# Performance work log

Measured on AMD Instinct MI355X. Metric: run time of the kernel, lower is better.

The kernel has to match this reference:

```python
import jax, jax.numpy as jnp
import numpy as np

N_NODES = 100000
N_EDGES = 1600000
IN_F = 16
C1, C2 = 32, 64
HID = 128
N_CLASSES = 10
NUM_LAYERS = 3


def setup_inputs() -> dict:
    key = jax.random.key(0)
    ks = jax.random.split(key, 20)
    s = 0.1
    inp = {
        "x": jax.random.normal(ks[0], (N_NODES, IN_F), dtype=jnp.float32),
        "edge_index": jax.random.randint(ks[1], (2, N_EDGES), 0, N_NODES, dtype=jnp.int64),
        "edge_attr": jax.random.uniform(ks[2], (N_EDGES, 1), dtype=jnp.float32),
        # conv1 (out=32): per-step weight [L, 32, 32], GRUCell params
        "W1": jax.random.normal(ks[3], (NUM_LAYERS, C1, C1), dtype=jnp.float32) * s,
        "Wih1": jax.random.normal(ks[4], (3 * C1, C1), dtype=jnp.float32) * s,
        "Whh1": jax.random.normal(ks[5], (3 * C1, C1), dtype=jnp.float32) * s,
        "bih1": jnp.zeros((3 * C1,), dtype=jnp.float32),
        "bhh1": jnp.zeros((3 * C1,), dtype=jnp.float32),
        # conv2 (out=64)
        "W2": jax.random.normal(ks[6], (NUM_LAYERS, C2, C2), dtype=jnp.float32) * s,
        "Wih2": jax.random.normal(ks[7], (3 * C2, C2), dtype=jnp.float32) * s,
        "Whh2": jax.random.normal(ks[8], (3 * C2, C2), dtype=jnp.float32) * s,
        "bih2": jnp.zeros((3 * C2,), dtype=jnp.float32),
        "bhh2": jnp.zeros((3 * C2,), dtype=jnp.float32),
        # MLP head
        "fc1_w": jax.random.normal(ks[9], (HID, C2), dtype=jnp.float32) * s,
        "fc1_b": jnp.zeros((HID,), dtype=jnp.float32),
        "fc2_w": jax.random.normal(ks[10], (N_CLASSES, HID), dtype=jnp.float32) * s,
        "fc2_b": jnp.zeros((N_CLASSES,), dtype=jnp.float32),
    }
    return inp


def _gru_cell(m, h, Wih, Whh, bih, bhh):
    gi = m @ Wih.T + bih
    gh = h @ Whh.T + bhh
    ir, iz, inn = jnp.split(gi, 3, axis=1)
    hr, hz, hn = jnp.split(gh, 3, axis=1)
    r = jax.nn.sigmoid(ir + hr)
    z = jax.nn.sigmoid(iz + hz)
    n = jnp.tanh(inn + r * hn)
    return (1.0 - z) * n + z * h


def _gated_graph_conv(x, edge_index, edge_weight, W, Wih, Whh, bih, bhh):
    # PyG GatedGraphConv with aggr='max'
    n, c = x.shape
    out_ch = W.shape[-1]
    h = jnp.pad(x, ((0, 0), (0, out_ch - c))) if c < out_ch else x
    src, dst = edge_index[0], edge_index[1]
    ew = edge_weight[:, None]
    for i in range(W.shape[0]):
        m = h @ W[i]
        msg = m[src] * ew                      # [E, out_ch] gather + scale
        agg = jax.ops.segment_max(msg, dst, num_segments=n)  # scatter-max
        agg = jnp.where(jnp.isfinite(agg), agg, 0.0)         # empty segs -> 0
        h = _gru_cell(agg, h, Wih, Whh, bih, bhh)
    return h


def reference(x, edge_index, edge_attr, W1, Wih1, Whh1, bih1, bhh1,
              W2, Wih2, Whh2, bih2, bhh2, fc1_w, fc1_b, fc2_w, fc2_b):
    ew = jnp.squeeze(edge_attr)
    h = jax.nn.elu(_gated_graph_conv(x, edge_index, ew, W1, Wih1, Whh1, bih1, bhh1))
    h = jax.nn.elu(_gated_graph_conv(h, edge_index, ew, W2, Wih2, Whh2, bih2, bhh2))
    h = jax.nn.elu(h @ fc1_w.T + fc1_b)
    logits = h @ fc2_w.T + fc2_b
    return jax.nn.log_softmax(logits, axis=1)
```

## Files before the change

### kernel.cpp

```cpp
#include <hip/hip_runtime.h>
#include <math.h>

#define N_NODES 100000
#define N_EDGES 1600000
#define SCAN_BS 1024
#define NBK 8
#define BKSH 14
#define NBINS (N_NODES*NBK)

typedef __attribute__((ext_vector_type(8))) short bf8_t;
typedef __attribute__((ext_vector_type(4))) float f4_t;
typedef unsigned short us;

__device__ __forceinline__ float sigmoidf_(float x){ return 1.f/(1.f + expf(-x)); }
__device__ __forceinline__ float eluf_(float x){ return x > 0.f ? x : expm1f(x); }
__device__ __forceinline__ us f2bf(float x){
  unsigned u = __float_as_uint(x);
  unsigned r = u + 0x7FFFu + ((u>>16)&1u);
  return (us)(r>>16);
}
__device__ __forceinline__ float bf2f(us v){
  return __uint_as_float(((unsigned)v)<<16);
}

__global__ void prep_all(const float* __restrict__ Wih1, const float* __restrict__ Whh1,
                         const float* __restrict__ Wih2, const float* __restrict__ Whh2,
                         const float* __restrict__ W1,   const float* __restrict__ W2,
                         const float* __restrict__ fc1w, const float* __restrict__ fc2w,
                         const float* __restrict__ fc2b,
                         us* Wihb1, us* Whhb1, us* Wihb2, us* Whhb2,
                         us* Wtb1, us* Wtb2, us* fc1wb, us* fc2wpb, float* fc2bp){
  int i = blockIdx.x*256 + threadIdx.x;
  if (i < 3072) { Wihb1[i]=f2bf(Wih1[i]); return; } i -= 3072;
  if (i < 3072) { Whhb1[i]=f2bf(Whh1[i]); return; } i -= 3072;
  if (i < 12288){ Wihb2[i]=f2bf(Wih2[i]); return; } i -= 12288;
  if (i < 12288){ Whhb2[i]=f2bf(Whh2[i]); return; } i -= 12288;
  if (i < 3072) { int k=i%32, c=(i/32)%32, m=i/1024;
                  Wtb1[i]=f2bf(W1[m*1024 + k*32 + c]); return; } i -= 3072;
  if (i < 12288){ int k=i%64, c=(i/64)%64, m=i/4096;
                  Wtb2[i]=f2bf(W2[m*4096 + k*64 + c]); return; } i -= 12288;
  if (i < 8192) { fc1wb[i]=f2bf(fc1w[i]); return; } i -= 8192;
  if (i < 2048) { int c=i/128, k=i%128;
                  fc2wpb[i]=(c<10)?f2bf(fc2w[c*128+k]):(us)0; return; } i -= 2048;
  if (i < 16)   { fc2bp[i] = (i<10)? fc2b[i] : 0.f; }
}

__global__ void zero_counts(int* cnt, int* cur, int n){
  int i = blockIdx.x*blockDim.x + threadIdx.x;
  if (i < n){ cnt[i]=0; cur[i]=0; }
}
__global__ void count_kernel(const int* __restrict__ ei, int* __restrict__ cnt, int e){
  int i = blockIdx.x*blockDim.x + threadIdx.x;
  if (i < e){
    int s = ei[i], d = ei[N_EDGES + i];
    atomicAdd(&cnt[d*NBK + (s>>BKSH)], 1);
  }
}
__global__ void scan1_kernel(const int* __restrict__ cnt, int* __restrict__ pre,
                             int* __restrict__ bsum, int n){
  __shared__ int sh[SCAN_BS];
  int t = threadIdx.x, gi = blockIdx.x*SCAN_BS + t;
  int v = (gi < n) ? cnt[gi] : 0;
  sh[t] = v;
  __syncthreads();
  for (int off=1; off<SCAN_BS; off<<=1){
    int u = (t>=off)?sh[t-off]:0;
    __syncthreads();
    sh[t] += u;
    __syncthreads();
  }
  if (gi < n) pre[gi] = sh[t] - v;
  if (t == SCAN_BS-1) bsum[blockIdx.x] = sh[t];
}
__global__ void scan2_kernel(int* __restrict__ bsum, int nb){
  __shared__ int sh[1024];
  int t = threadIdx.x;
  int v = (t < nb) ? bsum[t] : 0;
  sh[t] = v;
  __syncthreads();
  for (int off=1; off<1024; off<<=1){
    int u = (t>=off)?sh[t-off]:0;
    __syncthreads();
    sh[t] += u;
    __syncthreads();
  }
  if (t < nb) bsum[t] = sh[t] - v;
}
__global__ void scan3_kernel(const int* __restrict__ pre, const int* __restrict__ bsum,
                             int* __restrict__ rs2, int total){
  int i = blockIdx.x*blockDim.x + threadIdx.x;
  if (i < total) rs2[i] = pre[i] + bsum[i/SCAN_BS];
  if (i == 0) rs2[total] = N_EDGES;
}
__global__ void scatter_kernel(const int* __restrict__ ei, const float* __restrict__ ea,
    const int* __restrict__ rs2, int* __restrict__ cur,
    long long* __restrict__ esrc, int e){
  int i0 = (blockIdx.x*blockDim.x + threadIdx.x)*2;
  #pragma unroll
  for (int j=0;j<2;j++){
    int i = i0 + j;
    if (i < e){
      int s = ei[i], d = ei[N_EDGES + i];
      int bin = d*NBK + (s>>BKSH);
      int p = rs2[bin] + atomicAdd(&cur[bin], 1);
      long long v = (long long)(unsigned)s
                  | ((long long)(unsigned)__float_as_int(ea[i]) << 32);
      __builtin_nontemporal_store(v, &esrc[p]);
    }
  }
}

__global__ void pad_x_kernel(const float* __restrict__ x, float* __restrict__ h,
                             us* __restrict__ hb, int n){
  int i = blockIdx.x*blockDim.x + threadIdx.x;
  if (i < n*32){
    int node = i >> 5, c = i & 31;
    float v = (c < 16) ? x[node*16 + c] : 0.f;
    h[i] = v;
    hb[i] = f2bf(v);
  }
}
__global__ void transition_kernel(const float* __restrict__ h1, float* __restrict__ h2,
                                  us* __restrict__ h2b, int n){
  int i = blockIdx.x*blockDim.x + threadIdx.x;
  if (i < n*64){
    int node = i >> 6, c = i & 63;
    float v = (c < 32) ? eluf_(h1[node*32 + c]) : 0.f;
    h2[i] = v;
    h2b[i] = f2bf(v);
  }
}

template<int C>
__global__ __launch_bounds__(256) void mgemm_mfma(const us* __restrict__ hb,
    const us* __restrict__ Wtb, us* __restrict__ mb, int n){
  constexpr int NT = C/16, KS = C/32;
  int l = threadIdx.x & 63, w = threadIdx.x >> 6;
  int mbase = blockIdx.x*64 + w*16;
  if (mbase >= n) return;
  int lr = l & 15, lk = (l >> 4)*8;
  f4_t acc[NT];
  #pragma unroll
  for (int t=0;t<NT;t++) acc[t] = f4_t{0.f,0.f,0.f,0.f};
  #pragma unroll
  for (int ks=0; ks<KS; ks++){
    int k0 = ks*32 + lk;
    bf8_t a = *(const bf8_t*)(hb + (size_t)(mbase+lr)*C + k0);
    #pragma unroll
    for (int t=0;t<NT;t++){
      bf8_t b = *(const bf8_t*)(Wtb + (size_t)(t*16+lr)*C + k0);
      acc[t] = __builtin_amdgcn_mfma_f32_16x16x32_bf16(a, b, acc[t], 0, 0, 0);
    }
  }
  int dr = (l>>4)*4;
  #pragma unroll
  for (int t=0;t<NT;t++){
    #pragma unroll
    for (int r=0;r<4;r++){
      int node = mbase + dr + r;
      if (node < n)
        mb[(size_t)node*C + t*16 + lr] = f2bf(acc[t][r]);
    }
  }
}

template<int C>
__global__ void agg_kernel(const us* __restrict__ mb, const int* __restrict__ rs2,
    const long long* __restrict__ esrc, us* __restrict__ aggb, int n_nodes){
  constexpr int GPN = C/8;
  int gid = blockIdx.x*blockDim.x + threadIdx.x;
  int nn = gid / GPN, g8 = gid % GPN;
  if (nn >= n_nodes) return;
  int s = rs2[nn*NBK], e = rs2[nn*NBK + NBK];
  float acc[8];
  #pragma unroll
  for (int j=0;j<8;j++) acc[j] = -__builtin_inff();
  const us* mbg = mb + g8*8;
  int i = s;
  for (; i+4<=e; i+=4){
    long long e0 = esrc[i], e1 = esrc[i+1], e2 = esrc[i+2], e3 = esrc[i+3];
    uint4 v0 = *(const uint4*)(mbg + (size_t)(unsigned)(e0 & 0xFFFFFFFF)*C);
    uint4 v1 = *(const uint4*)(mbg + (size_t)(unsigned)(e1 & 0xFFFFFFFF)*C);
    uint4 v2 = *(const uint4*)(mbg + (size_t)(unsigned)(e2 & 0xFFFFFFFF)*C);
    uint4 v3 = *(const uint4*)(mbg + (size_t)(unsigned)(e3 & 0xFFFFFFFF)*C);
    float w0 = __int_as_float((int)(e0>>32)), w1 = __int_as_float((int)(e1>>32));
    float w2 = __int_as_float((int)(e2>>32)), w3 = __int_as_float((int)(e3>>32));
    unsigned a0[4] = {v0.x, v0.y, v0.z, v0.w};
    unsigned a1[4] = {v1.x, v1.y, v1.z, v1.w};
    unsigned a2[4] = {v2.x, v2.y, v2.z, v2.w};
    unsigned a3[4] = {v3.x, v3.y, v3.z, v3.w};
    #pragma unroll
    for (int q=0;q<4;q++){
      float x0 = fmaxf(__uint_as_float(a0[q]<<16)*w0, __uint_as_float(a1[q]<<16)*w1);
      float x1 = fmaxf(__uint_as_float(a2[q]<<16)*w2, __uint_as_float(a3[q]<<16)*w3);
      float y0 = fmaxf(__uint_as_float(a0[q]&0xFFFF0000u)*w0, __uint_as_float(a1[q]&0xFFFF0000u)*w1);
      float y1 = fmaxf(__uint_as_float(a2[q]&0xFFFF0000u)*w2, __uint_as_float(a3[q]&0xFFFF0000u)*w3);
      acc[2*q]   = fmaxf(acc[2*q],   fmaxf(x0, x1));
      acc[2*q+1] = fmaxf(acc[2*q+1], fmaxf(y0, y1));
    }
  }
  for (; i<e; i++){
    long long e0 = esrc[i];
    uint4 v0 = *(const uint4*)(mbg + (size_t)(unsigned)(e0 & 0xFFFFFFFF)*C);
    float w0 = __int_as_float((int)(e0>>32));
    unsigned a0[4] = {v0.x, v0.y, v0.z, v0.w};
    #pragma unroll
    for (int q=0;q<4;q++){
      acc[2*q]   = fmaxf(acc[2*q],   __uint_as_float(a0[q]<<16)*w0);
      acc[2*q+1] = fmaxf(acc[2*q+1], __uint_as_float(a0[q]&0xFFFF0000u)*w0);
    }
  }
  unsigned r[8];
  #pragma unroll
  for (int j=0;j<8;j++) r[j] = (e > s) ? (unsigned)f2bf(acc[j]) : 0u;
  uint4 o;
  o.x = r[0] | (r[1]<<16); o.y = r[2] | (r[3]<<16);
  o.z = r[4] | (r[5]<<16); o.w = r[6] | (r[7]<<16);
  *(uint4*)(aggb + (size_t)nn*C + g8*8) = o;
}

template<int C, bool COMPUTE_M>
__global__ __launch_bounds__(256) void gru_mfma(
    const us* __restrict__ aggb, const us* __restrict__ hbin,
    const float* __restrict__ hfin,
    const us* __restrict__ Wihb, const us* __restrict__ Whhb,
    const float* __restrict__ bih, const float* __restrict__ bhh,
    const us* __restrict__ Wtb_next,
    float* __restrict__ hfout, us* __restrict__ hbout, us* __restrict__ mbout, int n){
  constexpr int NT = 3*C/16;
  constexpr int KS = C/32;
  constexpr int CT = C/16;
  constexpr int TST = C + 8;
  constexpr int TSZ = COMPUTE_M ? 16*TST : 1;
  __shared__ us tlds[4][TSZ];
  int l = threadIdx.x & 63, w = threadIdx.x >> 6;
  int mbase = blockIdx.x*64 + w*16;
  int lr = l & 15, lk = (l >> 4)*8;
  f4_t accI[NT], accH[NT];
  #pragma unroll
  for (int t=0;t<NT;t++){ accI[t]=f4_t{0.f,0.f,0.f,0.f}; accH[t]=f4_t{0.f,0.f,0.f,0.f}; }
  #pragma unroll
  for (int ks=0; ks<KS; ks++){
    int k0 = ks*32 + lk;
    bf8_t aI = *(const bf8_t*)(aggb + (size_t)(mbase+lr)*C + k0);
    bf8_t aH = *(const bf8_t*)(hbin + (size_t)(mbase+lr)*C + k0);
    #pragma unroll
    for (int t=0;t<NT;t++){
      bf8_t bI = *(const bf8_t*)(Wihb + (size_t)(t*16+lr)*C + k0);
      accI[t] = __builtin_amdgcn_mfma_f32_16x16x32_bf16(aI, bI, accI[t], 0, 0, 0);
      bf8_t bH = *(const bf8_t*)(Whhb + (size_t)(t*16+lr)*C + k0);
      accH[t] = __builtin_amdgcn_mfma_f32_16x16x32_bf16(aH, bH, accH[t], 0, 0, 0);
    }
  }
  int dr = (l>>4)*4;
  us* tile = tlds[w];
  #pragma unroll
  for (int ct=0; ct<CT; ct++){
    int c = ct*16 + lr;
    float bR = bih[c],     cR = bhh[c];
    float bZ = bih[c+C],   cZ = bhh[c+C];
    float bN = bih[c+2*C], cN = bhh[c+2*C];
    #pragma unroll
    for (int r=0;r<4;r++){
      int i = mbase + dr + r;
      float giR = accI[ct][r] + bR,      ghR = accH[ct][r] + cR;
      float giZ = accI[CT+ct][r] + bZ,   ghZ = accH[CT+ct][r] + cZ;
      float giN = accI[2*CT+ct][r] + bN, ghN = accH[2*CT+ct][r] + cN;
      float rr = sigmoidf_(giR + ghR);
      float z  = sigmoidf_(giZ + ghZ);
      float nn = tanhf(giN + rr*ghN);
      float h  = hfin[(size_t)i*C + c];
      float ho = (1.f - z)*nn + z*h;
      us hob = f2bf(ho);
      if constexpr (COMPUTE_M)
        tile[(dr+r)*TST + c] = hob;
      if (i < n){
        hfout[(size_t)i*C + c] = ho;
        hbout[(size_t)i*C + c] = hob;
      }
    }
  }
  if constexpr (COMPUTE_M){
    __syncthreads();
    f4_t macc[CT];
    #pragma unroll
    for (int t=0;t<CT;t++) macc[t] = f4_t{0.f,0.f,0.f,0.f};
    #pragma unroll
    for (int ks=0; ks<KS; ks++){
      int k0 = ks*32 + lk;
      bf8_t a = *(const bf8_t*)(tile + lr*TST + k0);
      #pragma unroll
      for (int t=0;t<CT;t++){
        bf8_t b = *(const bf8_t*)(Wtb_next + (size_t)(t*16+lr)*C + k0);
        macc[t] = __builtin_amdgcn_mfma_f32_16x16x32_bf16(a, b, macc[t], 0, 0, 0);
      }
    }
    #pragma unroll
    for (int t=0;t<CT;t++){
      #pragma unroll
      for (int r=0;r<4;r++){
        int node = mbase + dr + r;
        if (node < n)
          mbout[(size_t)node*C + t*16 + lr] = f2bf(macc[t][r]);
      }
    }
  }
}

__global__ __launch_bounds__(256) void head_mfma(const float* __restrict__ h2,
    const us* __restrict__ fc1wb, const float* __restrict__ fc1b,
    const us* __restrict__ fc2wpb, const float* __restrict__ fc2bp,
    float* __restrict__ out, int n){
  __shared__ __align__(16) us lds[4][16*136];
  int l = threadIdx.x & 63, w = threadIdx.x >> 6;
  int mbase = blockIdx.x*64 + w*16;
  int lr = l & 15, lk = (l >> 4)*8;
  int dr = (l>>4)*4;
  f4_t acc1[8];
  #pragma unroll
  for (int t=0;t<8;t++) acc1[t] = f4_t{0.f,0.f,0.f,0.f};
  #pragma unroll
  for (int ks=0; ks<2; ks++){
    int k0 = ks*32 + lk;
    const float* hp = h2 + (size_t)(mbase+lr)*64 + k0;
    float4 v0 = *(const float4*)hp;
    float4 v1 = *(const float4*)(hp+4);
    bf8_t a;
    a[0]=(short)f2bf(eluf_(v0.x)); a[1]=(short)f2bf(eluf_(v0.y));
    a[2]=(short)f2bf(eluf_(v0.z)); a[3]=(short)f2bf(eluf_(v0.w));
    a[4]=(short)f2bf(eluf_(v1.x)); a[5]=(short)f2bf(eluf_(v1.y));
    a[6]=(short)f2bf(eluf_(v1.z)); a[7]=(short)f2bf(eluf_(v1.w));
    #pragma unroll
    for (int t=0;t<8;t++){
      bf8_t b = *(const bf8_t*)(fc1wb + (size_t)(t*16+lr)*64 + k0);
      acc1[t] = __builtin_amdgcn_mfma_f32_16x16x32_bf16(a, b, acc1[t], 0, 0, 0);
    }
  }
  us* tile = lds[w];
  #pragma unroll
  for (int t=0;t<8;t++){
    float b1 = fc1b[t*16 + lr];
    #pragma unroll
    for (int r=0;r<4;r++)
      tile[(dr+r)*136 + t*16 + lr] = f2bf(eluf_(acc1[t][r] + b1));
  }
  __syncthreads();
  f4_t acc2 = f4_t{0.f,0.f,0.f,0.f};
  #pragma unroll
  for (int ks=0; ks<4; ks++){
    int k0 = ks*32 + lk;
    bf8_t a = *(const bf8_t*)(tile + lr*136 + k0);
    bf8_t b = *(const bf8_t*)(fc2wpb + (size_t)lr*128 + k0);
    acc2 = __builtin_amdgcn_mfma_f32_16x16x32_bf16(a, b, acc2, 0, 0, 0);
  }
  float b2 = fc2bp[lr];
  #pragma unroll
  for (int r=0;r<4;r++){
    float val = acc2[r] + b2;
    float vm = (lr < 10) ? val : -__builtin_inff();
    #pragma unroll
    for (int m=1;m<16;m<<=1) vm = fmaxf(vm, __shfl_xor(vm, m, 64));
    float ex = (lr < 10) ? expf(val - vm) : 0.f;
    #pragma unroll
    for (int m=1;m<16;m<<=1) ex += __shfl_xor(ex, m, 64);
    float lse = vm + logf(ex);
    int node = mbase + dr + r;
    if (lr < 10 && node < n) out[(size_t)node*10 + lr] = val - lse;
  }
}

extern "C" void kernel_launch(void* const* d_in, const int* in_sizes, int n_in,
                              void* d_out, int out_size, void* d_ws, size_t ws_size,
                              hipStream_t stream){
  const float* x    = (const float*)d_in[0];
  const int*   ei   = (const int*)  d_in[1];
  const float* ea   = (const float*)d_in[2];
  const float* W1   = (const float*)d_in[3];
  const float* Wih1 = (const float*)d_in[4];
  const float* Whh1 = (const float*)d_in[5];
  const float* bih1 = (const float*)d_in[6];
  const float* bhh1 = (const float*)d_in[7];
  const float* W2   = (const float*)d_in[8];
  const float* Wih2 = (const float*)d_in[9];
  const float* Whh2 = (const float*)d_in[10];
  const float* bih2 = (const float*)d_in[11];
  const float* bhh2 = (const float*)d_in[12];
  const float* fc1w = (const float*)d_in[13];
  const float* fc1b = (const float*)d_in[14];
  const float* fc2w = (const float*)d_in[15];
  const float* fc2b = (const float*)d_in[16];
  float* outp = (float*)d_out;

  char* ws = (char*)d_ws;
  size_t off = 0;
  auto alloc = [&](size_t bytes)->void*{
    void* p = ws + off;
    off += (bytes + 255) & ~size_t(255);
    return p;
  };
  float* hA   = (float*)alloc(sizeof(float)*N_NODES*32);
  float* hB   = (float*)alloc(sizeof(float)*N_NODES*64);
  us* hAb0    = (us*)alloc(sizeof(us)*N_NODES*32);
  us* hAb1    = (us*)alloc(sizeof(us)*N_NODES*32);
  us* hBb0    = (us*)alloc(sizeof(us)*N_NODES*64);
  us* hBb1    = (us*)alloc(sizeof(us)*N_NODES*64);
  us* mb      = (us*)alloc(sizeof(us)*N_NODES*64);
  us* aggb    = (us*)alloc(sizeof(us)*N_NODES*64);
  int* rs2    = (int*)alloc(sizeof(int)*(NBINS+1));
  int* cnt    = (int*)alloc(sizeof(int)*NBINS);
  int* cur    = (int*)alloc(sizeof(int)*NBINS);
  int* pre    = (int*)alloc(sizeof(int)*NBINS);
  int* bsum   = (int*)alloc(sizeof(int)*1024);
  long long* esrc = (long long*)alloc(sizeof(long long)*N_EDGES);
  us* Wihb1   = (us*)alloc(sizeof(us)*96*32);
  us* Whhb1   = (us*)alloc(sizeof(us)*96*32);
  us* Wihb2   = (us*)alloc(sizeof(us)*192*64);
  us* Whhb2   = (us*)alloc(sizeof(us)*192*64);
  us* Wtb1    = (us*)alloc(sizeof(us)*3*32*32);
  us* Wtb2    = (us*)alloc(sizeof(us)*3*64*64);
  us* fc1wb   = (us*)alloc(sizeof(us)*128*64);
  us* fc2wpb  = (us*)alloc(sizeof(us)*16*128);
  float* fc2bp= (float*)alloc(sizeof(float)*16);
  (void)ws_size; (void)in_sizes; (void)n_in; (void)out_size;

  const int n = N_NODES, e = N_EDGES;
  const int nbk = (NBINS + SCAN_BS - 1)/SCAN_BS;
  const int gblk = (n + 63)/64;

  prep_all<<<(56336+255)/256,256,0,stream>>>(Wih1, Whh1, Wih2, Whh2, W1, W2,
      fc1w, fc2w, fc2b, Wihb1, Whhb1, Wihb2, Whhb2, Wtb1, Wtb2, fc1wb, fc2wpb, fc2bp);

  zero_counts<<<(NBINS+255)/256,256,0,stream>>>(cnt, cur, NBINS);
  count_kernel<<<(e+255)/256,256,0,stream>>>(ei, cnt, e);
  scan1_kernel<<<nbk,SCAN_BS,0,stream>>>(cnt, pre, bsum, NBINS);
  scan2_kernel<<<1,1024,0,stream>>>(bsum, nbk);
  scan3_kernel<<<(NBINS+255)/256,256,0,stream>>>(pre, bsum, rs2, NBINS);
  scatter_kernel<<<(e/2+255)/256,256,0,stream>>>(ei, ea, rs2, cur, esrc, e);

  pad_x_kernel<<<(n*32+255)/256,256,0,stream>>>(x, hA, hAb0, n);
  {
    us* c0 = hAb0; us* c1 = hAb1;
    mgemm_mfma<32><<<gblk,256,0,stream>>>(c0, Wtb1, mb, n);
    for (int i=0;i<3;i++){
      agg_kernel<32><<<((long long)n*4+255)/256,256,0,stream>>>(mb, rs2, esrc, aggb, n);
      if (i < 2)
        gru_mfma<32,true><<<gblk,256,0,stream>>>(aggb, c0, hA, Wihb1, Whhb1, bih1, bhh1,
                                                 Wtb1 + (i+1)*32*32, hA, c1, mb, n);
      else
        gru_mfma<32,false><<<gblk,256,0,stream>>>(aggb, c0, hA, Wihb1, Whhb1, bih1, bhh1,
                                                  nullptr, hA, c1, nullptr, n);
      us* t = c0; c0 = c1; c1 = t;
    }
  }

  transition_kernel<<<(n*64+255)/256,256,0,stream>>>(hA, hB, hBb0, n);

  {
    us* c0 = hBb0; us* c1 = hBb1;
    mgemm_mfma<64><<<gblk,256,0,stream>>>(c0, Wtb2, mb, n);
    for (int i=0;i<3;i++){
      agg_kernel<64><<<((long long)n*8+255)/256,256,0,stream>>>(mb, rs2, esrc, aggb, n);
      if (i < 2)
        gru_mfma<64,true><<<gblk,256,0,stream>>>(aggb, c0, hB, Wihb2, Whhb2, bih2, bhh2,
                                                 Wtb2 + (i+1)*64*64, hB, c1, mb, n);
      else
        gru_mfma<64,false><<<gblk,256,0,stream>>>(aggb, c0, hB, Wihb2, Whhb2, bih2, bhh2,
                                                  nullptr, hB, c1, nullptr, n);
      us* t = c0; c0 = c1; c1 = t;
    }
  }

  head_mfma<<<gblk,256,0,stream>>>(hB, fc1wb, fc1b, fc2wpb, fc2bp, outp, n);
}
```

Measured before the change: 675.0 us.

## Pre-partition edges by destination range before CSR scatter to localize atomics

```diff
diff --git a/kernel.cpp b/kernel.cpp
--- a/kernel.cpp
+++ b/kernel.cpp
@@ -7,10 +7,13 @@
 #define NBK 8
 #define BKSH 14
 #define NBINS (N_NODES*NBK)
+#define NPART 196
+#define PCAP 1536
 
 typedef __attribute__((ext_vector_type(8))) short bf8_t;
 typedef __attribute__((ext_vector_type(4))) float f4_t;
 typedef unsigned short us;
+typedef unsigned long long ull;
 
 __device__ __forceinline__ float sigmoidf_(float x){ return 1.f/(1.f + expf(-x)); }
 __device__ __forceinline__ float eluf_(float x){ return x > 0.f ? x : expm1f(x); }
@@ -45,15 +48,27 @@
   if (i < 16)   { fc2bp[i] = (i<10)? fc2b[i] : 0.f; }
 }
 
-__global__ void zero_counts(int* cnt, int* cur, int n){
+__global__ void zero_counts(int* cnt, int* cur, int n, int* pcur, int np){
   int i = blockIdx.x*blockDim.x + threadIdx.x;
   if (i < n){ cnt[i]=0; cur[i]=0; }
-}
-__global__ void count_kernel(const int* __restrict__ ei, int* __restrict__ cnt, int e){
-  int i = blockIdx.x*blockDim.x + threadIdx.x;
-  if (i < e){
-    int s = ei[i], d = ei[N_EDGES + i];
-    atomicAdd(&cnt[d*NBK + (s>>BKSH)], 1);
+  if (i < np) pcur[i]=0;
+}
+__global__ void part_kernel(const int* __restrict__ ei, const float* __restrict__ ea,
+    int* __restrict__ cnt, int* __restrict__ pcur, ull* __restrict__ pbuf, int e){
+  int i0 = (blockIdx.x*blockDim.x + threadIdx.x)*2;
+  int xcd = blockIdx.x & 7;
+  #pragma unroll
+  for (int j=0;j<2;j++){
+    int i = i0 + j;
+    if (i < e){
+      int s = ei[i], d = ei[N_EDGES + i];
+      atomicAdd(&cnt[d*NBK + (s>>BKSH)], 1);
+      unsigned ew16 = f2bf(ea[i]);
+      int slot = xcd*NPART + (d>>9);
+      int pos = atomicAdd(&pcur[slot], 1);
+      pbuf[(size_t)slot*PCAP + pos] =
+          (ull)(unsigned)s | ((ull)(unsigned)d << 17) | ((ull)ew16 << 34);
+    }
   }
 }
 __global__ void scan1_kernel(const int* __restrict__ cnt, int* __restrict__ pre,
@@ -92,20 +107,22 @@
   if (i < total) rs2[i] = pre[i] + bsum[i/SCAN_BS];
   if (i == 0) rs2[total] = N_EDGES;
 }
-__global__ void scatter_kernel(const int* __restrict__ ei, const float* __restrict__ ea,
-    const int* __restrict__ rs2, int* __restrict__ cur,
-    long long* __restrict__ esrc, int e){
-  int i0 = (blockIdx.x*blockDim.x + threadIdx.x)*2;
-  #pragma unroll
-  for (int j=0;j<2;j++){
-    int i = i0 + j;
-    if (i < e){
-      int s = ei[i], d = ei[N_EDGES + i];
-      int bin = d*NBK + (s>>BKSH);
-      int p = rs2[bin] + atomicAdd(&cur[bin], 1);
-      long long v = (long long)(unsigned)s
-                  | ((long long)(unsigned)__float_as_int(ea[i]) << 32);
-      __builtin_nontemporal_store(v, &esrc[p]);
+__global__ void scatter2_kernel(const ull* __restrict__ pbuf, const int* __restrict__ pcur,
+    const int* __restrict__ rs2, int* __restrict__ cur, ull* __restrict__ esrc){
+  int p = blockIdx.x >> 1;
+  int xlo = (blockIdx.x & 1)*4;
+  for (int x=xlo; x<xlo+4; x++){
+    int slot = x*NPART + p;
+    int len = pcur[slot];
+    const ull* seg = pbuf + (size_t)slot*PCAP;
+    for (int i=threadIdx.x; i<len; i+=256){
+      ull v = seg[i];
+      int src = (int)(v & 0x1FFFFu);
+      int dst = (int)((v>>17) & 0x1FFFFu);
+      unsigned ew16 = (unsigned)((v>>34) & 0xFFFFu);
+      int bin = dst*NBK + (src>>BKSH);
+      int pos = rs2[bin] + atomicAdd(&cur[bin], 1);
+      esrc[pos] = (ull)(unsigned)src | ((ull)(ew16<<16) << 32);
     }
   }
 }
@@ -166,7 +183,7 @@
 
 template<int C>
 __global__ void agg_kernel(const us* __restrict__ mb, const int* __restrict__ rs2,
-    const long long* __restrict__ esrc, us* __restrict__ aggb, int n_nodes){
+    const ull* __restrict__ esrc, us* __restrict__ aggb, int n_nodes){
   constexpr int GPN = C/8;
   int gid = blockIdx.x*blockDim.x + threadIdx.x;
   int nn = gid / GPN, g8 = gid % GPN;
@@ -178,7 +195,7 @@
   const us* mbg = mb + g8*8;
   int i = s;
   for (; i+4<=e; i+=4){
-    long long e0 = esrc[i], e1 = esrc[i+1], e2 = esrc[i+2], e3 = esrc[i+3];
+    ull e0 = esrc[i], e1 = esrc[i+1], e2 = esrc[i+2], e3 = esrc[i+3];
     uint4 v0 = *(const uint4*)(mbg + (size_t)(unsigned)(e0 & 0xFFFFFFFF)*C);
     uint4 v1 = *(const uint4*)(mbg + (size_t)(unsigned)(e1 & 0xFFFFFFFF)*C);
     uint4 v2 = *(const uint4*)(mbg + (size_t)(unsigned)(e2 & 0xFFFFFFFF)*C);
@@ -200,7 +217,7 @@
     }
   }
   for (; i<e; i++){
-    long long e0 = esrc[i];
+    ull e0 = esrc[i];
     uint4 v0 = *(const uint4*)(mbg + (size_t)(unsigned)(e0 & 0xFFFFFFFF)*C);
     float w0 = __int_as_float((int)(e0>>32));
     unsigned a0[4] = {v0.x, v0.y, v0.z, v0.w};
@@ -411,7 +428,9 @@
   int* cur    = (int*)alloc(sizeof(int)*NBINS);
   int* pre    = (int*)alloc(sizeof(int)*NBINS);
   int* bsum   = (int*)alloc(sizeof(int)*1024);
-  long long* esrc = (long long*)alloc(sizeof(long long)*N_EDGES);
+  ull* esrc   = (ull*)alloc(sizeof(ull)*N_EDGES);
+  ull* pbuf   = (ull*)alloc(sizeof(ull)*8*NPART*PCAP);
+  int* pcur   = (int*)alloc(sizeof(int)*8*NPART);
   us* Wihb1   = (us*)alloc(sizeof(us)*96*32);
   us* Whhb1   = (us*)alloc(sizeof(us)*96*32);
   us* Wihb2   = (us*)alloc(sizeof(us)*192*64);
@@ -430,12 +449,12 @@
   prep_all<<<(56336+255)/256,256,0,stream>>>(Wih1, Whh1, Wih2, Whh2, W1, W2,
       fc1w, fc2w, fc2b, Wihb1, Whhb1, Wihb2, Whhb2, Wtb1, Wtb2, fc1wb, fc2wpb, fc2bp);
 
-  zero_counts<<<(NBINS+255)/256,256,0,stream>>>(cnt, cur, NBINS);
-  count_kernel<<<(e+255)/256,256,0,stream>>>(ei, cnt, e);
+  zero_counts<<<(NBINS+255)/256,256,0,stream>>>(cnt, cur, NBINS, pcur, 8*NPART);
+  part_kernel<<<(e/2+255)/256,256,0,stream>>>(ei, ea, cnt, pcur, pbuf, e);
   scan1_kernel<<<nbk,SCAN_BS,0,stream>>>(cnt, pre, bsum, NBINS);
   scan2_kernel<<<1,1024,0,stream>>>(bsum, nbk);
   scan3_kernel<<<(NBINS+255)/256,256,0,stream>>>(pre, bsum, rs2, NBINS);
-  scatter_kernel<<<(e/2+255)/256,256,0,stream>>>(ei, ea, rs2, cur, esrc, e);
+  scatter2_kernel<<<NPART*2,256,0,stream>>>(pbuf, pcur, rs2, cur, esrc);
 
   pad_x_kernel<<<(n*32+255)/256,256,0,stream>>>(x, hA, hAb0, n);
   {
```

Result: slower. 837.7 us (+24.1%).
